# Performance work log

Hardware: AMD Instinct MI355X
Metric: run time of the kernel (lower is better)

## Reference

```python
import jax, jax.numpy as jnp
import numpy as np

EPS = 1e-5

def _layer_norm(x, g, b):
    mu = jnp.mean(x, axis=-1, keepdims=True)
    var = jnp.mean(jnp.square(x - mu), axis=-1, keepdims=True)
    return (x - mu) * jax.lax.rsqrt(var + EPS) * g + b

def setup_inputs() -> dict:
    key = jax.random.key(0)
    Bsz, N, H = 2, 384, 128
    ks = jax.random.split(key, 16)
    s = 1.0 / np.sqrt(H)
    d = {
        'h_nodes': jax.random.normal(ks[0], (Bsz, N, H), jnp.float32),
        'h_edges': jax.random.normal(ks[1], (Bsz, N, N, H), jnp.float32),
        'adj_matrix_mask': (jax.random.uniform(ks[2], (Bsz, N, N)) < 0.5).astype(jnp.float32),
    }
    for i, nm in enumerate(['U', 'V', 'A', 'B', 'C']):
        d[nm + '_w'] = jax.random.normal(ks[3 + 2 * i], (H, H), jnp.float32) * s
        d[nm + '_b'] = jax.random.normal(ks[4 + 2 * i], (H,), jnp.float32) * s
    d['gh'] = jnp.ones((H,), jnp.float32); d['bh'] = jnp.zeros((H,), jnp.float32)
    d['ge'] = jnp.ones((H,), jnp.float32); d['be'] = jnp.zeros((H,), jnp.float32)
    return d

def reference(h_nodes, h_edges, adj_matrix_mask, U_w, U_b, V_w, V_b, A_w, A_b, B_w, B_b, C_w, C_b, gh, bh, ge, be):
    # torch Linear: y = x @ W^T + b
    Uh = h_nodes @ U_w.T + U_b            # [B,N,H]
    Vh = h_nodes @ V_w.T + V_b            # [B,N,H] (j features)
    Ah = h_nodes @ A_w.T + A_b
    Bh = h_nodes @ B_w.T + B_b
    Ce = h_edges @ C_w.T + C_b            # [B,N,N,H]
    e_upd = Ah[:, :, None, :] + Bh[:, None, :, :] + Ce   # [B,N,N,H]
    gates = jax.nn.sigmoid(e_upd)
    msgs = gates * Vh[:, None, :, :] * adj_matrix_mask[..., None]
    agg = jnp.sum(msgs, axis=2)           # sum over j -> [B,N,H]
    h_upd = jax.nn.relu(_layer_norm(Uh + agg, gh, bh))
    e_act = jax.nn.relu(_layer_norm(e_upd, ge, be))
    return (h_nodes + h_upd, h_edges + e_act)
```

## Files before the change

### kernel.cpp

```cpp
#include <hip/hip_runtime.h>
#include <hip/hip_bf16.h>

typedef __bf16 bf16_t;
typedef __bf16 bf16x8 __attribute__((ext_vector_type(8)));
typedef __bf16 bf16x4 __attribute__((ext_vector_type(4)));
typedef float f32x4 __attribute__((ext_vector_type(4)));

#define HD 128
#define NN 384
#define ROWS 768
#define SZ 98304
#define JC 6

__device__ inline int detect_f32(const void* p) {
    const unsigned short* u = (const unsigned short*)p;
    int bad = 0;
    #pragma unroll
    for (int k = 0; k < 128; ++k) {
        int e = (u[k] >> 7) & 0xFF;
        bad += (e < 110 || e > 135) ? 1 : 0;
    }
    return bad >= 16 ? 1 : 0;
}

__global__ __launch_bounds__(64) void detect_kernel(const void* p, float* ws) {
    if (threadIdx.x == 0)
        *(int*)((char*)ws + (size_t)10 * SZ * 4) = detect_f32(p);
}

__device__ inline int read_flag(const float* ws) {
    return *(const int*)((const char*)ws + (size_t)10 * SZ * 4);
}

template<int CTRL>
__device__ __attribute__((always_inline)) inline float dpp_add(float x) {
    int xi = __builtin_bit_cast(int, x);
    int yi = __builtin_amdgcn_update_dpp(0, xi, CTRL, 0xF, 0xF, true);
    return x + __builtin_bit_cast(float, yi);
}
__device__ __attribute__((always_inline)) inline float row16_sum(float x) {
    x = dpp_add<0xB1>(x);
    x = dpp_add<0x4E>(x);
    x = dpp_add<0x124>(x);
    x = dpp_add<0x128>(x);
    return x;
}

__device__ __attribute__((always_inline)) inline void ld8(const float* p, float* o) {
    f32x4 a = *(const f32x4*)p;
    f32x4 b = *(const f32x4*)(p + 4);
    o[0] = a[0]; o[1] = a[1]; o[2] = a[2]; o[3] = a[3];
    o[4] = b[0]; o[5] = b[1]; o[6] = b[2]; o[7] = b[3];
}
__device__ __attribute__((always_inline)) inline void ld8(const bf16_t* p, float* o) {
    bf16x8 v = *(const bf16x8*)p;
    #pragma unroll
    for (int e = 0; e < 8; ++e) o[e] = (float)v[e];
}
__device__ __attribute__((always_inline)) inline bf16x8 ld8b(const float* p) {
    f32x4 a = *(const f32x4*)p;
    f32x4 b = *(const f32x4*)(p + 4);
    bf16x8 v;
    #pragma unroll
    for (int e = 0; e < 4; ++e) { v[e] = (bf16_t)a[e]; v[e + 4] = (bf16_t)b[e]; }
    return v;
}
__device__ __attribute__((always_inline)) inline bf16x8 ld8b(const bf16_t* p) { return *(const bf16x8*)p; }
__device__ __attribute__((always_inline)) inline bf16x4 ld4b(const float* p) {
    f32x4 a = *(const f32x4*)p;
    bf16x4 v;
    #pragma unroll
    for (int e = 0; e < 4; ++e) v[e] = (bf16_t)a[e];
    return v;
}
__device__ __attribute__((always_inline)) inline bf16x4 ld4b(const bf16_t* p) { return *(const bf16x4*)p; }

template<typename T>
__device__ void node_body(float* x,
    const T* h_nodes, const T* Uw, const T* Ub, const T* Vw, const T* Vb,
    const T* Aw, const T* Ab, const T* Bw, const T* Bb, const T* Cb,
    float* ws)
{
    const int row = blockIdx.x, m = blockIdx.y, t = threadIdx.x;
    x[t] = (float)h_nodes[row * HD + t];
    __syncthreads();

    const T* Ws[4] = {Aw, Bw, Vw, Uw};
    float bias;
    if (m == 0)      bias = (float)Ab[t] + (float)Cb[t];
    else if (m == 1) bias = (float)Bb[t];
    else if (m == 2) bias = (float)Vb[t];
    else             bias = (float)Ub[t];

    float acc = bias;
    const T* W = Ws[m] + (size_t)t * HD;
    #pragma unroll
    for (int kk = 0; kk < 16; ++kk) {
        float w8[8];
        ld8(W + kk * 8, w8);
        #pragma unroll
        for (int e = 0; e < 8; ++e) acc = fmaf(x[kk * 8 + e], w8[e], acc);
    }
    ws[m * SZ + row * HD + t] = acc;
}

__global__ __launch_bounds__(128) void node_linear(
    const void* h_nodes, const void* Uw, const void* Ub, const void* Vw, const void* Vb,
    const void* Aw, const void* Ab, const void* Bw, const void* Bb, const void* Cb,
    float* __restrict__ ws)
{
    __shared__ __align__(16) float x[HD];
    if (read_flag(ws))
        node_body<float>(x, (const float*)h_nodes, (const float*)Uw, (const float*)Ub,
                         (const float*)Vw, (const float*)Vb, (const float*)Aw, (const float*)Ab,
                         (const float*)Bw, (const float*)Bb, (const float*)Cb, ws);
    else
        node_body<bf16_t>(x, (const bf16_t*)h_nodes, (const bf16_t*)Uw, (const bf16_t*)Ub,
                          (const bf16_t*)Vw, (const bf16_t*)Vb, (const bf16_t*)Aw, (const bf16_t*)Ab,
                          (const bf16_t*)Bw, (const bf16_t*)Bb, (const bf16_t*)Cb, ws);
}

struct Smem {
    bf16_t sCw[128 * 128];
    float sAhC[HD], sGe[HD], sBe[HD];
    float sAgg[4][HD];
};

template<typename T>
__device__ void edge_body(Smem& sm,
    const T* __restrict__ h_edges, const T* __restrict__ adj,
    const T* __restrict__ Cw, const T* __restrict__ ge, const T* __restrict__ be,
    const float* __restrict__ ws, float* __restrict__ wagg, float* __restrict__ out)
{
    const int i = blockIdx.x, jc = blockIdx.y, b = blockIdx.z;
    const int bi = b * NN + i;
    const int t = threadIdx.x;
    const int l = t & 63, w = t >> 6;
    const int lr = l & 15, lg = l >> 4;
    const int hbase = lg * 4;

    {
        const int slot = t & 15;
        #pragma unroll
        for (int p = 0; p < 8; ++p) {
            const int row = p * 16 + (t >> 4);
            bf16x8 v = ld8b(&Cw[(size_t)row * HD + slot * 8]);
            *(bf16x8*)((char*)sm.sCw + row * 256 + ((slot ^ (row & 15)) << 4)) = v;
        }
    }
    if (t < HD) {
        sm.sAhC[t] = ws[0 * SZ + bi * HD + t];
        sm.sGe[t]  = (float)ge[t];
        sm.sBe[t]  = (float)be[t];
    }

    __syncthreads();

    const T* Ebase = h_edges + (size_t)bi * NN * HD;
    const int j = jc * 64 + w * 16 + lr;
    const T* Erow = &Ebase[(size_t)j * HD];

    const float mk = (float)adj[(size_t)bi * NN + j];
    bf16x4 res[8];
    #pragma unroll
    for (int ct = 0; ct < 8; ++ct)
        res[ct] = ld4b(&Erow[ct * 16 + hbase]);

    const float* Bhrow = ws + 1 * SZ + ((size_t)b * NN + j) * HD;
    const float* Vhrow = ws + 2 * SZ + ((size_t)b * NN + j) * HD;
    f32x4 bhv[8], vhv[8];
    #pragma unroll
    for (int ct = 0; ct < 8; ++ct) {
        bhv[ct] = *(const f32x4*)&Bhrow[ct * 16 + hbase];
        vhv[ct] = *(const f32x4*)&Vhrow[ct * 16 + hbase];
    }

    f32x4 acc[8];
    #pragma unroll
    for (int ct = 0; ct < 8; ++ct) acc[ct] = (f32x4){0.f, 0.f, 0.f, 0.f};
    #pragma unroll
    for (int ks = 0; ks < 4; ++ks) {
        bf16x8 a = ld8b(&Erow[ks * 32 + lg * 8]);
        #pragma unroll
        for (int ct = 0; ct < 8; ++ct) {
            bf16x8 Bf = *(const bf16x8*)((const char*)sm.sCw +
                          (ct * 16 + lr) * 256 + ((((ks << 2) | lg) ^ lr) << 4));
            acc[ct] = __builtin_amdgcn_mfma_f32_16x16x32_bf16(Bf, a, acc[ct], 0, 0, 0);
        }
    }

    float* Orow = out + SZ + ((size_t)bi * NN + j) * HD;

    float sum = 0.f, ssq = 0.f;
    #pragma unroll
    for (int ct = 0; ct < 8; ++ct) {
        f32x4 e = acc[ct];
        f32x4 av = *(const f32x4*)&sm.sAhC[ct * 16 + hbase];
        e = e + av + bhv[ct];
        acc[ct] = e;
        #pragma unroll
        for (int r = 0; r < 4; ++r) { sum += e[r]; ssq = fmaf(e[r], e[r], ssq); }
    }
    sum += __shfl_xor(sum, 16); ssq += __shfl_xor(ssq, 16);
    sum += __shfl_xor(sum, 32); ssq += __shfl_xor(ssq, 32);
    const float mean = sum * (1.f / HD);
    const float rstd = rsqrtf(ssq * (1.f / HD) - mean * mean + 1e-5f);

    f32x4 agg4[8];
    #pragma unroll
    for (int ct = 0; ct < 8; ++ct) {
        f32x4 ge4 = *(const f32x4*)&sm.sGe[ct * 16 + hbase];
        f32x4 be4 = *(const f32x4*)&sm.sBe[ct * 16 + hbase];
        f32x4 o;
        #pragma unroll
        for (int r = 0; r < 4; ++r) {
            const float ee = acc[ct][r];
            const float g = 1.f / (1.f + exp2f(ee * -1.44269504f));
            agg4[ct][r] = g * mk * vhv[ct][r];
            float a = (ee - mean) * rstd;
            a = fmaf(a, ge4[r], be4[r]);
            a = fmaxf(a, 0.f);
            o[r] = (float)res[ct][r] + a;
        }
        *(f32x4*)&Orow[ct * 16 + hbase] = o;
    }

    #pragma unroll
    for (int ct = 0; ct < 8; ++ct)
        #pragma unroll
        for (int r = 0; r < 4; ++r)
            agg4[ct][r] = row16_sum(agg4[ct][r]);
    if (lr == 0) {
        #pragma unroll
        for (int ct = 0; ct < 8; ++ct)
            *(f32x4*)&sm.sAgg[w][ct * 16 + hbase] = agg4[ct];
    }
    __syncthreads();

    if (t < HD) {
        float p = sm.sAgg[0][t] + sm.sAgg[1][t] + sm.sAgg[2][t] + sm.sAgg[3][t];
        wagg[((size_t)jc * ROWS + bi) * HD + t] = p;
    }
}

__global__ __launch_bounds__(256) void edge_kernel(
    const void* h_edges, const void* adj, const void* Cw,
    const void* ge, const void* be,
    float* __restrict__ ws, float* __restrict__ out)
{
    __shared__ Smem sm;
    float* wagg = ws + 4 * SZ;
    if (read_flag(ws))
        edge_body<float>(sm, (const float*)h_edges, (const float*)adj, (const float*)Cw,
                         (const float*)ge, (const float*)be, ws, wagg, out);
    else
        edge_body<bf16_t>(sm, (const bf16_t*)h_edges, (const bf16_t*)adj, (const bf16_t*)Cw,
                          (const bf16_t*)ge, (const bf16_t*)be, ws, wagg, out);
}

template<typename T>
__device__ void node_upd_body(const T* h_nodes, const T* gh, const T* bh,
                              const float* ws, float* out)
{
    const int bi = blockIdx.x, t = threadIdx.x;
    float x0 = ws[3 * SZ + bi * HD + t];
    float x1 = ws[3 * SZ + bi * HD + t + 64];
    #pragma unroll
    for (int jc = 0; jc < JC; ++jc) {
        const float* p = ws + 4 * SZ + ((size_t)jc * ROWS + bi) * HD;
        x0 += p[t];
        x1 += p[t + 64];
    }
    float sum = x0 + x1;
    float ssq = x0 * x0 + x1 * x1;
    #pragma unroll
    for (int off = 1; off < 64; off <<= 1) {
        sum += __shfl_xor(sum, off);
        ssq += __shfl_xor(ssq, off);
    }
    const float mean = sum * (1.f / HD);
    const float rstd = rsqrtf(ssq * (1.f / HD) - mean * mean + 1e-5f);
    float a0 = fmaf((x0 - mean) * rstd, (float)gh[t],      (float)bh[t]);
    float a1 = fmaf((x1 - mean) * rstd, (float)gh[t + 64], (float)bh[t + 64]);
    a0 = fmaxf(a0, 0.f);
    a1 = fmaxf(a1, 0.f);
    out[bi * HD + t]      = (float)h_nodes[bi * HD + t]      + a0;
    out[bi * HD + t + 64] = (float)h_nodes[bi * HD + t + 64] + a1;
}

__global__ __launch_bounds__(64) void node_update(
    const void* h_nodes, const void* gh, const void* bh,
    const float* __restrict__ ws, float* __restrict__ out)
{
    if (read_flag(ws))
        node_upd_body<float>((const float*)h_nodes, (const float*)gh, (const float*)bh, ws, out);
    else
        node_upd_body<bf16_t>((const bf16_t*)h_nodes, (const bf16_t*)gh, (const bf16_t*)bh, ws, out);
}

extern "C" void kernel_launch(void* const* d_in, const int* in_sizes, int n_in,
                              void* d_out, int out_size, void* d_ws, size_t ws_size,
                              hipStream_t stream)
{
    float* ws = (float*)d_ws;
    float* out = (float*)d_out;

    detect_kernel<<<dim3(1), dim3(64), 0, stream>>>(d_in[0], ws);
    node_linear<<<dim3(ROWS, 4), dim3(128), 0, stream>>>(
        d_in[0], d_in[3], d_in[4], d_in[5], d_in[6], d_in[7], d_in[8],
        d_in[9], d_in[10], d_in[12], ws);
    edge_kernel<<<dim3(NN, JC, 2), dim3(256), 0, stream>>>(
        d_in[1], d_in[2], d_in[11], d_in[15], d_in[16], ws, out);
    node_update<<<dim3(ROWS), dim3(64), 0, stream>>>(
        d_in[0], d_in[13], d_in[14], ws, out);
}
```

Measured before the change: 145.7 us.

## Process two j-rows per lane in edge kernel to halve chunk count

Each wave now handles 32 edge rows (two 16-row MFMA tiles) instead of 16, so JC drops from 6 to 3 and the per-block Cw shared-memory staging is amortised over twice the work. The B-fragment read from LDS is reused for two MFMAs, and the partial aggregate is accumulated over both row groups before the cross-lane reduction. The workspace flag offset moves because fewer partial-aggregate slots are needed. This costs more registers per thread and halves the grid, which may reduce occupancy and latency hiding.

Measured after the change: 165.1 us. 13.3% more time.

```diff
diff --git a/kernel.cpp b/kernel.cpp
--- a/kernel.cpp
+++ b/kernel.cpp
@@ -10,7 +10,7 @@
 #define NN 384
 #define ROWS 768
 #define SZ 98304
-#define JC 6
+#define JC 3
 
 __device__ inline int detect_f32(const void* p) {
     const unsigned short* u = (const unsigned short*)p;
@@ -25,11 +25,11 @@
 
 __global__ __launch_bounds__(64) void detect_kernel(const void* p, float* ws) {
     if (threadIdx.x == 0)
-        *(int*)((char*)ws + (size_t)10 * SZ * 4) = detect_f32(p);
+        *(int*)((char*)ws + (size_t)7 * SZ * 4) = detect_f32(p);
 }
 
 __device__ inline int read_flag(const float* ws) {
-    return *(const int*)((const char*)ws + (size_t)10 * SZ * 4);
+    return *(const int*)((const char*)ws + (size_t)7 * SZ * 4);
 }
 
 template<int CTRL>
@@ -157,72 +157,130 @@
     __syncthreads();
 
     const T* Ebase = h_edges + (size_t)bi * NN * HD;
-    const int j = jc * 64 + w * 16 + lr;
-    const T* Erow = &Ebase[(size_t)j * HD];
-
-    const float mk = (float)adj[(size_t)bi * NN + j];
-    bf16x4 res[8];
+    const int j0 = jc * 128 + w * 32;
+    const int jA = j0 + lr, jB = j0 + 16 + lr;
+    const T* ErowA = &Ebase[(size_t)jA * HD];
+    const T* ErowB = &Ebase[(size_t)jB * HD];
+
+    const float mkA = (float)adj[(size_t)bi * NN + jA];
+    const float mkB = (float)adj[(size_t)bi * NN + jB];
+    bf16x4 resA[8];
     #pragma unroll
     for (int ct = 0; ct < 8; ++ct)
-        res[ct] = ld4b(&Erow[ct * 16 + hbase]);
-
-    const float* Bhrow = ws + 1 * SZ + ((size_t)b * NN + j) * HD;
-    const float* Vhrow = ws + 2 * SZ + ((size_t)b * NN + j) * HD;
-    f32x4 bhv[8], vhv[8];
+        resA[ct] = ld4b(&ErowA[ct * 16 + hbase]);
+    const float* BhA = ws + 1 * SZ + ((size_t)b * NN + jA) * HD;
+    const float* VhA = ws + 2 * SZ + ((size_t)b * NN + jA) * HD;
+    f32x4 bhvA[8], vhvA[8];
     #pragma unroll
     for (int ct = 0; ct < 8; ++ct) {
-        bhv[ct] = *(const f32x4*)&Bhrow[ct * 16 + hbase];
-        vhv[ct] = *(const f32x4*)&Vhrow[ct * 16 + hbase];
-    }
-
-    f32x4 acc[8];
-    #pragma unroll
-    for (int ct = 0; ct < 8; ++ct) acc[ct] = (f32x4){0.f, 0.f, 0.f, 0.f};
+        bhvA[ct] = *(const f32x4*)&BhA[ct * 16 + hbase];
+        vhvA[ct] = *(const f32x4*)&VhA[ct * 16 + hbase];
+    }
+
+    f32x4 acc0[8], acc1[8];
+    #pragma unroll
+    for (int ct = 0; ct < 8; ++ct) {
+        acc0[ct] = (f32x4){0.f, 0.f, 0.f, 0.f};
+        acc1[ct] = (f32x4){0.f, 0.f, 0.f, 0.f};
+    }
     #pragma unroll
     for (int ks = 0; ks < 4; ++ks) {
-        bf16x8 a = ld8b(&Erow[ks * 32 + lg * 8]);
+        bf16x8 a0 = ld8b(&ErowA[ks * 32 + lg * 8]);
+        bf16x8 a1 = ld8b(&ErowB[ks * 32 + lg * 8]);
         #pragma unroll
         for (int ct = 0; ct < 8; ++ct) {
             bf16x8 Bf = *(const bf16x8*)((const char*)sm.sCw +
                           (ct * 16 + lr) * 256 + ((((ks << 2) | lg) ^ lr) << 4));
-            acc[ct] = __builtin_amdgcn_mfma_f32_16x16x32_bf16(Bf, a, acc[ct], 0, 0, 0);
-        }
-    }
-
-    float* Orow = out + SZ + ((size_t)bi * NN + j) * HD;
-
-    float sum = 0.f, ssq = 0.f;
+            acc0[ct] = __builtin_amdgcn_mfma_f32_16x16x32_bf16(Bf, a0, acc0[ct], 0, 0, 0);
+            acc1[ct] = __builtin_amdgcn_mfma_f32_16x16x32_bf16(Bf, a1, acc1[ct], 0, 0, 0);
+        }
+    }
+
+    bf16x4 resB[8];
+    #pragma unroll
+    for (int ct = 0; ct < 8; ++ct)
+        resB[ct] = ld4b(&ErowB[ct * 16 + hbase]);
+    const float* BhB = ws + 1 * SZ + ((size_t)b * NN + jB) * HD;
+    const float* VhB = ws + 2 * SZ + ((size_t)b * NN + jB) * HD;
+    f32x4 bhvB[8], vhvB[8];
     #pragma unroll
     for (int ct = 0; ct < 8; ++ct) {
-        f32x4 e = acc[ct];
-        f32x4 av = *(const f32x4*)&sm.sAhC[ct * 16 + hbase];
-        e = e + av + bhv[ct];
-        acc[ct] = e;
-        #pragma unroll
-        for (int r = 0; r < 4; ++r) { sum += e[r]; ssq = fmaf(e[r], e[r], ssq); }
-    }
-    sum += __shfl_xor(sum, 16); ssq += __shfl_xor(ssq, 16);
-    sum += __shfl_xor(sum, 32); ssq += __shfl_xor(ssq, 32);
-    const float mean = sum * (1.f / HD);
-    const float rstd = rsqrtf(ssq * (1.f / HD) - mean * mean + 1e-5f);
+        bhvB[ct] = *(const f32x4*)&BhB[ct * 16 + hbase];
+        vhvB[ct] = *(const f32x4*)&VhB[ct * 16 + hbase];
+    }
 
     f32x4 agg4[8];
     #pragma unroll
-    for (int ct = 0; ct < 8; ++ct) {
-        f32x4 ge4 = *(const f32x4*)&sm.sGe[ct * 16 + hbase];
-        f32x4 be4 = *(const f32x4*)&sm.sBe[ct * 16 + hbase];
-        f32x4 o;
-        #pragma unroll
-        for (int r = 0; r < 4; ++r) {
-            const float ee = acc[ct][r];
-            const float g = 1.f / (1.f + exp2f(ee * -1.44269504f));
-            agg4[ct][r] = g * mk * vhv[ct][r];
-            float a = (ee - mean) * rstd;
-            a = fmaf(a, ge4[r], be4[r]);
-            a = fmaxf(a, 0.f);
-            o[r] = (float)res[ct][r] + a;
-        }
-        *(f32x4*)&Orow[ct * 16 + hbase] = o;
+    for (int ct = 0; ct < 8; ++ct) agg4[ct] = (f32x4){0.f, 0.f, 0.f, 0.f};
+
+    {
+        float* Orow = out + SZ + ((size_t)bi * NN + jA) * HD;
+        float sum = 0.f, ssq = 0.f;
+        #pragma unroll
+        for (int ct = 0; ct < 8; ++ct) {
+            f32x4 e = acc0[ct];
+            f32x4 av = *(const f32x4*)&sm.sAhC[ct * 16 + hbase];
+            e = e + av + bhvA[ct];
+            acc0[ct] = e;
+            #pragma unroll
+            for (int r = 0; r < 4; ++r) { sum += e[r]; ssq = fmaf(e[r], e[r], ssq); }
+        }
+        sum += __shfl_xor(sum, 16); ssq += __shfl_xor(ssq, 16);
+        sum += __shfl_xor(sum, 32); ssq += __shfl_xor(ssq, 32);
+        const float mean = sum * (1.f / HD);
+        const float rstd = rsqrtf(ssq * (1.f / HD) - mean * mean + 1e-5f);
+        #pragma unroll
+        for (int ct = 0; ct < 8; ++ct) {
+            f32x4 ge4 = *(const f32x4*)&sm.sGe[ct * 16 + hbase];
+            f32x4 be4 = *(const f32x4*)&sm.sBe[ct * 16 + hbase];
+            f32x4 o;
+            #pragma unroll
+            for (int r = 0; r < 4; ++r) {
+                const float ee = acc0[ct][r];
+                const float g = 1.f / (1.f + exp2f(ee * -1.44269504f));
+                agg4[ct][r] = fmaf(g * mkA, vhvA[ct][r], agg4[ct][r]);
+                float a = (ee - mean) * rstd;
+                a = fmaf(a, ge4[r], be4[r]);
+                a = fmaxf(a, 0.f);
+                o[r] = (float)resA[ct][r] + a;
+            }
+            *(f32x4*)&Orow[ct * 16 + hbase] = o;
+        }
+    }
+
+    {
+        float* Orow = out + SZ + ((size_t)bi * NN + jB) * HD;
+        float sum = 0.f, ssq = 0.f;
+        #pragma unroll
+        for (int ct = 0; ct < 8; ++ct) {
+            f32x4 e = acc1[ct];
+            f32x4 av = *(const f32x4*)&sm.sAhC[ct * 16 + hbase];
+            e = e + av + bhvB[ct];
+            acc1[ct] = e;
+            #pragma unroll
+            for (int r = 0; r < 4; ++r) { sum += e[r]; ssq = fmaf(e[r], e[r], ssq); }
+        }
+        sum += __shfl_xor(sum, 16); ssq += __shfl_xor(ssq, 16);
+        sum += __shfl_xor(sum, 32); ssq += __shfl_xor(ssq, 32);
+        const float mean = sum * (1.f / HD);
+        const float rstd = rsqrtf(ssq * (1.f / HD) - mean * mean + 1e-5f);
+        #pragma unroll
+        for (int ct = 0; ct < 8; ++ct) {
+            f32x4 ge4 = *(const f32x4*)&sm.sGe[ct * 16 + hbase];
+            f32x4 be4 = *(const f32x4*)&sm.sBe[ct * 16 + hbase];
+            f32x4 o;
+            #pragma unroll
+            for (int r = 0; r < 4; ++r) {
+                const float ee = acc1[ct][r];
+                const float g = 1.f / (1.f + exp2f(ee * -1.44269504f));
+                agg4[ct][r] = fmaf(g * mkB, vhvB[ct][r], agg4[ct][r]);
+                float a = (ee - mean) * rstd;
+                a = fmaf(a, ge4[r], be4[r]);
+                a = fmaxf(a, 0.f);
+                o[r] = (float)resB[ct][r] + a;
+            }
+            *(f32x4*)&Orow[ct * 16 + hbase] = o;
+        }
     }
 
     #pragma unroll
```
